# Kernel tuning notes

Hardware: AMD Instinct MI355X
Metric: run time of the kernel (lower is better)

The kernel has to match this reference:

```python
import jax, jax.numpy as jnp
import numpy as np
import math

H = 8        # num_heads
DK = 64      # key_dim
DV = 64      # value_dim
FACTOR = 4


def setup_inputs() -> dict:
    key = jax.random.key(0)
    B, T, S, D = 4, 2048, 2048, 512
    Dout = H * DV
    ks = jax.random.split(key, 16)
    sample_k = min(int(FACTOR * math.log(S)), S)  # = 33
    inp = {
        "x_q": jax.random.normal(ks[0], (B, T, D), jnp.float32),
        "x_k": jax.random.normal(ks[1], (B, S, D), jnp.float32),
        "x_v": jax.random.normal(ks[2], (B, S, D), jnp.float32),
        "Wq": jax.random.normal(ks[3], (D, H * DK), jnp.float32) * 0.02,
        "bq": jnp.zeros((H * DK,), jnp.float32),
        "Wk": jax.random.normal(ks[4], (D, H * DK), jnp.float32) * 0.02,
        "bk": jnp.zeros((H * DK,), jnp.float32),
        "Wv": jax.random.normal(ks[5], (D, H * DV), jnp.float32) * 0.02,
        "bv": jnp.zeros((H * DV,), jnp.float32),
        "Wo": jax.random.normal(ks[6], (H * DV, Dout), jnp.float32) * 0.02,
        "bo": jnp.zeros((Dout,), jnp.float32),
        "index_sample": jax.random.randint(ks[7], (T, sample_k), 0, S, jnp.int32),
    }
    return inp


def reference(x_q, x_k, x_v, Wq, bq, Wk, bk, Wv, bv, Wo, bo, index_sample):
    B, T, D = x_q.shape
    S = x_k.shape[1]
    u = min(int(FACTOR * math.log(T)), T)  # n_top queries kept

    q = (x_q @ Wq + bq).reshape(B, T, H, DK)
    k = (x_k @ Wk + bk).reshape(B, S, H, DK)
    v = (x_v @ Wv + bv).reshape(B, S, H, DV)

    # --- _prob_QK: sampled QK to score queries ---
    ks = k[:, index_sample]                                  # [B,T,J,H,dk]
    qk_s = jnp.einsum('bthd,btjhd->bthj', q, ks)             # [B,T,H,J]
    M = qk_s.max(-1) - qk_s.mean(-1)                         # [B,T,H]
    _, top = jax.lax.top_k(jnp.transpose(M, (0, 2, 1)), u)   # [B,H,u]

    b_idx = jnp.arange(B)[:, None, None]
    h_idx = jnp.arange(H)[None, :, None]
    q_red = q[b_idx, top, h_idx]                             # [B,H,u,dk]
    qk = jnp.einsum('bhud,bshd->bhus', q_red, k)             # [B,H,u,S]

    # --- s0: default (no mask) context = mean of values over S ---
    ctx = jnp.broadcast_to(v.mean(axis=1, keepdims=True), (B, T, H, DV))
    ctx = jnp.transpose(ctx, (0, 2, 1, 3))                   # [B,H,T,dv]

    # --- s1: scaled softmax over full keys for top queries ---
    scores = jax.nn.softmax(qk * (1.0 / math.sqrt(DK)), axis=-1)
    attn = jnp.einsum('bhus,bshd->bhud', scores, v)          # [B,H,u,dv]

    # --- scatter top-query results into context / scores ---
    ctx = ctx.at[b_idx, h_idx, top].set(attn)                # [B,H,T,dv]
    final_scores = jnp.full((B, H, T, S), 1.0 / S, dtype=scores.dtype)
    final_scores = final_scores.at[b_idx, h_idx, top].set(scores)

    out = jnp.transpose(ctx, (0, 2, 1, 3)).reshape(B, T, H * DV)
    out = out @ Wo + bo                                      # [B,T,output_dim]
    return out, final_scores
```

## Files before the change

### kernel.cpp

```cpp
#include <hip/hip_runtime.h>

typedef __attribute__((ext_vector_type(8))) short short8;
typedef __attribute__((ext_vector_type(4))) float f32x4;

constexpr int Bn  = 4;
constexpr int Tn  = 2048;
constexpr int Sn  = 2048;
constexpr int Dn  = 512;
constexpr int Hn  = 8;
constexpr int DKn = 64;
constexpr int DVn = 64;
constexpr int HDn = 512;
constexpr int SKn = 30;
constexpr int Un  = 30;
constexpr int Gu  = 6;
constexpr int NGroups = Un / Gu;
constexpr int NAttnG  = Bn * Hn * NGroups;
constexpr int NOutF   = (Bn * Tn) / 8;
constexpr int RowSplit = 57344;
constexpr int NGemm  = 768;
constexpr int NFillA = RowSplit / 4;
constexpr int NTailF = (Bn * Hn * Tn - RowSplit) / 4;
constexpr float kScale = 0.125f;

constexpr int NWsplit = 192;
constexpr int NVPart  = 64;

__device__ __forceinline__ ushort bf16_rne(float x) {
  unsigned u = __float_as_uint(x);
  return (ushort)((u + 0x7fffu + ((u >> 16) & 1u)) >> 16);
}
__device__ __forceinline__ float bf16f(ushort h) {
  return __uint_as_float(((unsigned)h) << 16);
}
__device__ __forceinline__ void nt_store4(f32x4* p, f32x4 v) {
  __builtin_nontemporal_store(v, p);
}

#define MFMA(accv, av, bv) \
  asm volatile("v_mfma_f32_16x16x32_bf16 %0, %1, %2, %0" : "+v"(accv) : "v"(av), "v"(bv))

__global__ __launch_bounds__(256) void prep_split_kernel(
    const float* __restrict__ Wq, const float* __restrict__ Wk, const float* __restrict__ Wv,
    ushort* __restrict__ WtH, ushort* __restrict__ WtL) {
  const int tid = threadIdx.x;
  const int bid = blockIdx.x;

  const int z = bid / 64, t = bid % 64;
  const int k0 = (t >> 3) * 64, n0 = (t & 7) * 64;
  const float* W = (z == 0) ? Wq : (z == 1) ? Wk : Wv;
  __shared__ float tile[64][65];
  const int r = tid >> 2, c0 = (tid & 3) * 16;
#pragma unroll
  for (int i = 0; i < 16; i += 4) {
    const float4 vv = *(const float4*)(W + (size_t)(k0 + r) * HDn + n0 + c0 + i);
    tile[r][c0 + i] = vv.x; tile[r][c0 + i + 1] = vv.y;
    tile[r][c0 + i + 2] = vv.z; tile[r][c0 + i + 3] = vv.w;
  }
  __syncthreads();
  unsigned hp[8], lp[8];
#pragma unroll
  for (int i = 0; i < 16; i += 2) {
    const float x0 = tile[c0 + i][r];
    const float x1 = tile[c0 + i + 1][r];
    const ushort h0 = bf16_rne(x0), h1 = bf16_rne(x1);
    const ushort l0 = bf16_rne(x0 - bf16f(h0)), l1 = bf16_rne(x1 - bf16f(h1));
    hp[i >> 1] = (unsigned)h0 | ((unsigned)h1 << 16);
    lp[i >> 1] = (unsigned)l0 | ((unsigned)l1 << 16);
  }
  const size_t off = (size_t)(z * 512 + n0 + r) * 512 + k0 + c0;
  *(uint4*)(WtH + off)     = make_uint4(hp[0], hp[1], hp[2], hp[3]);
  *(uint4*)(WtH + off + 8) = make_uint4(hp[4], hp[5], hp[6], hp[7]);
  *(uint4*)(WtL + off)     = make_uint4(lp[0], lp[1], lp[2], lp[3]);
  *(uint4*)(WtL + off + 8) = make_uint4(lp[4], lp[5], lp[6], lp[7]);
}

__global__ __launch_bounds__(256, 2) void gemm_fill_kernel(
    const float* __restrict__ xq, const float* __restrict__ xk, const float* __restrict__ xv,
    const ushort* __restrict__ WtH, const ushort* __restrict__ WtL,
    const float* __restrict__ bq, const float* __restrict__ bk, const float* __restrict__ bv,
    float* __restrict__ qo, float* __restrict__ ko, float* __restrict__ vo,
    float* __restrict__ fscores) {
  const int bid = blockIdx.x;
  const int tid = threadIdx.x;

  if (bid >= NGemm) {
    const size_t r0 = (size_t)(bid - NGemm) * 4;
    const float c = 1.0f / Sn;
    const f32x4 c4v = {c, c, c, c};
    f32x4* fs4 = (f32x4*)fscores + r0 * (Sn / 4);
#pragma unroll
    for (int i = 0; i < 8; ++i) nt_store4(fs4 + i * 256 + tid, c4v);
    return;
  }

  __shared__ ushort AsH[64][32];
  __shared__ ushort AsL[64][32];
  __shared__ ushort BsH[256][32];
  __shared__ ushort BsL[256][32];

  const int z = bid >> 8;
  const int rem = bid & 255;
  const int bm = (rem >> 1) * 64;
  const int bn = (rem & 1) * 256;
  const float* X = (z == 0) ? xq : (z == 1) ? xk : xv;
  const float* bias = (z == 0) ? bq : (z == 1) ? bk : bv;
  float* Y = (z == 0) ? qo : (z == 1) ? ko : vo;

  const int lane = tid & 63;
  const int wave = tid >> 6;
  const int fr = lane & 15;
  const int gk = lane >> 4;

  const int ar = tid >> 2, ag = tid & 3;
  const float* xrow = X + (size_t)(bm + ar) * Dn + ag * 8;
  const int brow0 = tid >> 2, bg = tid & 3;
  const ushort* wh = WtH + (size_t)(z * 512 + bn + brow0) * 512 + bg * 8;
  const ushort* wl = WtL + (size_t)(z * 512 + bn + brow0) * 512 + bg * 8;

  f32x4 acc[4][4];
#pragma unroll
  for (int m = 0; m < 4; ++m)
#pragma unroll
    for (int n = 0; n < 4; ++n)
#pragma unroll
      for (int j = 0; j < 4; ++j) acc[m][n][j] = 0.f;

  float4 af0, af1;
  uint4 sbH[4], sbL[4];
#define STG_LOAD(k0_) do { \
    af0 = *(const float4*)(xrow + (k0_)); \
    af1 = *(const float4*)(xrow + (k0_) + 4); \
    sbH[0] = *(const uint4*)(wh + (k0_));          sbL[0] = *(const uint4*)(wl + (k0_)); \
    sbH[1] = *(const uint4*)(wh + (k0_) + 32768);  sbL[1] = *(const uint4*)(wl + (k0_) + 32768); \
    sbH[2] = *(const uint4*)(wh + (k0_) + 65536);  sbL[2] = *(const uint4*)(wl + (k0_) + 65536); \
    sbH[3] = *(const uint4*)(wh + (k0_) + 98304);  sbL[3] = *(const uint4*)(wl + (k0_) + 98304); \
  } while (0)

  const int agq = (ag ^ ((ar >> 1) & 3)) * 8;
  const int bgx = bg ^ ((brow0 >> 1) & 3);
  const int gq = (gk ^ ((fr >> 1) & 3)) * 8;

  STG_LOAD(0);
  for (int k0 = 0; k0 < Dn; k0 += 32) {
    __syncthreads();
    {
      float xf[8] = {af0.x, af0.y, af0.z, af0.w, af1.x, af1.y, af1.z, af1.w};
      unsigned hp[4], lp[4];
#pragma unroll
      for (int i = 0; i < 8; i += 2) {
        const ushort h0 = bf16_rne(xf[i]), h1 = bf16_rne(xf[i + 1]);
        const ushort l0 = bf16_rne(xf[i] - bf16f(h0)), l1 = bf16_rne(xf[i + 1] - bf16f(h1));
        hp[i >> 1] = (unsigned)h0 | ((unsigned)h1 << 16);
        lp[i >> 1] = (unsigned)l0 | ((unsigned)l1 << 16);
      }
      *(uint4*)&AsH[ar][agq] = make_uint4(hp[0], hp[1], hp[2], hp[3]);
      *(uint4*)&AsL[ar][agq] = make_uint4(lp[0], lp[1], lp[2], lp[3]);
#pragma unroll
      for (int p = 0; p < 4; ++p) {
        const int n = brow0 + p * 64;
        *(uint4*)&BsH[n][bgx * 8] = sbH[p];
        *(uint4*)&BsL[n][bgx * 8] = sbL[p];
      }
    }
    __syncthreads();
    if (k0 + 32 < Dn) STG_LOAD(k0 + 32);

    short8 aH[4], aL[4], bH[4], bL[4];
#pragma unroll
    for (int m = 0; m < 4; ++m) {
      aH[m] = *(const short8*)&AsH[m * 16 + fr][gq];
      aL[m] = *(const short8*)&AsL[m * 16 + fr][gq];
    }
#pragma unroll
    for (int n = 0; n < 4; ++n) {
      bH[n] = *(const short8*)&BsH[wave * 64 + n * 16 + fr][gq];
      bL[n] = *(const short8*)&BsL[wave * 64 + n * 16 + fr][gq];
    }
#pragma unroll
    for (int m = 0; m < 4; ++m)
#pragma unroll
      for (int n = 0; n < 4; ++n) {
        MFMA(acc[m][n], aH[m], bH[n]);
        MFMA(acc[m][n], aH[m], bL[n]);
        MFMA(acc[m][n], aL[m], bH[n]);
      }
  }
  asm volatile("s_nop 7\n\ts_nop 7");

  float bsv[4];
#pragma unroll
  for (int n = 0; n < 4; ++n) bsv[n] = bias[bn + wave * 64 + n * 16 + fr];
#pragma unroll
  for (int m = 0; m < 4; ++m) {
#pragma unroll
    for (int n = 0; n < 4; ++n) {
      const int col = bn + wave * 64 + n * 16 + fr;
#pragma unroll
      for (int j = 0; j < 4; ++j) {
        Y[(size_t)(bm + m * 16 + gk * 4 + j) * HDn + col] = acc[m][n][j] + bsv[n];
      }
    }
  }
#undef STG_LOAD
}

__global__ __launch_bounds__(64) void sampled_m_kernel(
    const float* __restrict__ q, const float* __restrict__ k,
    const int* __restrict__ idxs, float* __restrict__ Mt,
    const float* __restrict__ v, float* __restrict__ vpart) {
  if (blockIdx.x >= Bn * Tn) {
    const int pb = blockIdx.x - Bn * Tn;
    const int b = pb >> 4, part = pb & 15;
    const int ln = threadIdx.x;
    const float4* v4 = (const float4*)(v + (size_t)b * Sn * HDn);
    float4 a0 = make_float4(0.f, 0.f, 0.f, 0.f);
    float4 a1 = make_float4(0.f, 0.f, 0.f, 0.f);
    const int s0 = part * 128;
    for (int s = s0; s < s0 + 128; ++s) {
      const float4 x0 = v4[(size_t)s * 128 + ln * 2];
      const float4 x1 = v4[(size_t)s * 128 + ln * 2 + 1];
      a0.x += x0.x; a0.y += x0.y; a0.z += x0.z; a0.w += x0.w;
      a1.x += x1.x; a1.y += x1.y; a1.z += x1.z; a1.w += x1.w;
    }
    float4* vp4 = (float4*)vpart + (size_t)pb * 128;
    vp4[ln * 2] = a0; vp4[ln * 2 + 1] = a1;
    return;
  }

  const int bt = blockIdx.x;
  const int b = bt >> 11, t = bt & (Tn - 1);
  const int lane = threadIdx.x;
  const int jq = lane >> 4;
  const int d16 = lane & 15;
  __shared__ int sidx[32];
  if (lane < SKn) sidx[lane] = idxs[t * SKn + lane];
  if (lane >= SKn && lane < 32) sidx[lane] = 0;
  __syncthreads();
  const float* qrow = q + (size_t)bt * HDn;
  const float* kb = k + (size_t)b * Sn * HDn;
  for (int h = 0; h < Hn; ++h) {
    const float4 qv = *(const float4*)(qrow + h * DKn + d16 * 4);
    float mx = -1e30f, sum = 0.f;
#pragma unroll
    for (int jb = 0; jb < 32; jb += 4) {
      const int j = jb + jq;
      const int srow = sidx[j];
      const float4 kv = *(const float4*)(kb + (size_t)srow * HDn + h * DKn + d16 * 4);
      float p = kv.x * qv.x + kv.y * qv.y + kv.z * qv.z + kv.w * qv.w;
      p += __shfl_xor(p, 1);
      p += __shfl_xor(p, 2);
      p += __shfl_xor(p, 4);
      p += __shfl_xor(p, 8);
      if (j < SKn) { mx = fmaxf(mx, p); sum += p; }
    }
    mx = fmaxf(mx, __shfl_xor(mx, 16));
    mx = fmaxf(mx, __shfl_xor(mx, 32));
    sum += __shfl_xor(sum, 16);
    sum += __shfl_xor(sum, 32);
    if (lane == 0) Mt[((size_t)(b * Hn + h)) * Tn + t] = mx - sum * (1.0f / SKn);
  }
}

__global__ __launch_bounds__(256) void topk_vmean_base_kernel(
    const float* __restrict__ Mt, const float* __restrict__ vpart,
    const float* __restrict__ Wo, const float* __restrict__ bo,
    int* __restrict__ top, float* __restrict__ vmean, float* __restrict__ basep) {
  const int tid = threadIdx.x;
  const int lane = tid & 63, w = tid >> 6;
  __shared__ float vals[Tn];
  __shared__ float wv[4];
  __shared__ int wi[4];
  __shared__ float4 part[256];
  __shared__ float vm[HDn];

  if (blockIdx.x < 32) {
    const int bh = blockIdx.x;
    for (int i = tid; i < Tn; i += 256) vals[i] = Mt[(size_t)bh * Tn + i];
    __syncthreads();
    for (int u = 0; u < Un; ++u) {
      float bv = -1e30f; int bi = 0x7fffffff;
      for (int i = tid; i < Tn; i += 256) {
        const float x = vals[i];
        if (x > bv) { bv = x; bi = i; }
      }
#pragma unroll
      for (int o = 1; o < 64; o <<= 1) {
        const float ov = __shfl_xor(bv, o);
        const int oi = __shfl_xor(bi, o);
        if (ov > bv || (ov == bv && oi < bi)) { bv = ov; bi = oi; }
      }
      if (lane == 0) { wv[w] = bv; wi[w] = bi; }
      __syncthreads();
      bv = wv[0]; bi = wi[0];
#pragma unroll
      for (int j = 1; j < 4; ++j) {
        if (wv[j] > bv || (wv[j] == bv && wi[j] < bi)) { bv = wv[j]; bi = wi[j]; }
      }
      if (tid == 0) { top[bh * Un + u] = bi; vals[bi] = -1e30f; }
      __syncthreads();
    }
  } else {
    const int b = blockIdx.x - 32;
    const int c4 = tid & 127, half = tid >> 7;
    float4 acc = make_float4(0.f, 0.f, 0.f, 0.f);
    for (int p = half * 8; p < half * 8 + 8; ++p) {
      const float4 x = ((const float4*)vpart)[(size_t)(b * 16 + p) * 128 + c4];
      acc.x += x.x; acc.y += x.y; acc.z += x.z; acc.w += x.w;
    }
    part[tid] = acc;
    __syncthreads();
    if (half == 0) {
      float4 a = part[c4], bpp = part[128 + c4];
      const float sc = 1.0f / Sn;
      float4 r = make_float4((a.x + bpp.x) * sc, (a.y + bpp.y) * sc,
                             (a.z + bpp.z) * sc, (a.w + bpp.w) * sc);
      *(float4*)(vm + c4 * 4) = r;
      *(float4*)(vmean + b * HDn + c4 * 4) = r;
    }
    __syncthreads();
    const float4* Wo4 = (const float4*)Wo;
    float4 acc2 = make_float4(0.f, 0.f, 0.f, 0.f);
    for (int c = half * 256; c < half * 256 + 256; ++c) {
      const float vmc = vm[c];
      const float4 wrow = Wo4[(size_t)c * 128 + c4];
      acc2.x += vmc * wrow.x; acc2.y += vmc * wrow.y;
      acc2.z += vmc * wrow.z; acc2.w += vmc * wrow.w;
    }
    __syncthreads();
    part[tid] = acc2;
    __syncthreads();
    if (half == 0) {
      float4 a = part[c4], bpp = part[128 + c4];
      const float4 bb = ((const float4*)bo)[c4];
      float4 r = make_float4(a.x + bpp.x + bb.x, a.y + bpp.y + bb.y,
                             a.z + bpp.z + bb.z, a.w + bpp.w + bb.w);
      ((float4*)basep)[b * 128 + c4] = r;
    }
  }
}

__global__ __launch_bounds__(256) void attn_out_kernel(
    const float* __restrict__ q, const float* __restrict__ k,
    const float* __restrict__ v, const float* __restrict__ vmean,
    const int* __restrict__ top, const float* __restrict__ Wo,
    const float* __restrict__ basep,
    float* __restrict__ out, float* __restrict__ fscores) {
  const int tid = threadIdx.x;
  const int bid = blockIdx.x;

  if (bid >= NAttnG + NOutF) {
    const int fid = bid - NAttnG - NOutF;
    const int r = RowSplit + fid * 4;
    const int bh = r >> 11;
    const int tbase = r & (Tn - 1);
    __shared__ int sflag4[4];
    if (tid < 4) sflag4[tid] = 0;
    __syncthreads();
    if (tid < Un) {
      const int d = top[bh * Un + tid] - tbase;
      if (d >= 0 && d < 4) sflag4[d] = 1;
    }
    __syncthreads();
    const float c = 1.0f / Sn;
    const f32x4 c4v = {c, c, c, c};
    f32x4* fs4 = (f32x4*)fscores + (size_t)r * (Sn / 4);
#pragma unroll
    for (int rr = 0; rr < 4; ++rr) {
      if (!sflag4[rr]) {
        f32x4* row = fs4 + rr * (Sn / 4);
        nt_store4(row + tid, c4v);
        nt_store4(row + 256 + tid, c4v);
      }
    }
    return;
  }

  if (bid >= NAttnG) {
    const int fid = bid - NAttnG;
    const int r0 = fid * 8;
    const int b = r0 >> 11;
    const int t0 = r0 & (Tn - 1);
    __shared__ int sflag8[8];
    if (tid < 8) sflag8[tid] = 0;
    __syncthreads();
    if (tid < Hn * Un) {
      const int d = top[b * Hn * Un + tid] - t0;
      if (d >= 0 && d < 8) sflag8[d] = 1;
    }
    __syncthreads();
    const int col4 = tid & 127, rh = tid >> 7;
    const float4 bv4 = ((const float4*)basep)[b * 128 + col4];
    const f32x4 bvx = {bv4.x, bv4.y, bv4.z, bv4.w};
#pragma unroll
    for (int rp = 0; rp < 4; ++rp) {
      const int rr = rp * 2 + rh;
      float4* orow4 = (float4*)(out + (size_t)(r0 + rr) * HDn) + col4;
      if (sflag8[rr]) {
        float* p = (float*)orow4;
        atomicAdd(p + 0, bv4.x); atomicAdd(p + 1, bv4.y);
        atomicAdd(p + 2, bv4.z); atomicAdd(p + 3, bv4.w);
      } else {
        nt_store4((f32x4*)orow4, bvx);
      }
    }
    return;
  }

  const int grp = bid % NGroups;
  const int bh = bid / NGroups;
  const int h = bh & (Hn - 1), b = bh >> 3;
  const int u0 = grp * Gu;
  const int lane = tid & 63, w = tid >> 6;

  __shared__ float qs[Gu][DKn];
  __shared__ float sc[Gu][2052];
  __shared__ float red[8];
  __shared__ int tsel[Gu];
  __shared__ float4 partv[4][Gu][16];

  if (tid < Gu) tsel[tid] = top[bh * Un + u0 + tid];
  __syncthreads();
  for (int i = tid; i < Gu * DKn; i += 256) {
    const int g = i >> 6, d = i & 63;
    qs[g][d] = q[((size_t)(b * Tn + tsel[g])) * HDn + h * DKn + d];
  }
  __syncthreads();

  const float4* k4 = (const float4*)k;
  for (int s = tid; s < Sn; s += 256) {
    const float4* krow = k4 + ((size_t)(b * Sn + s)) * 128 + h * 16;
    float acc[Gu];
#pragma unroll
    for (int g = 0; g < Gu; ++g) acc[g] = 0.f;
#pragma unroll
    for (int d4i = 0; d4i < 16; ++d4i) {
      const float4 kv = krow[d4i];
#pragma unroll
      for (int g = 0; g < Gu; ++g) {
        const float4 qv = *(const float4*)&qs[g][d4i * 4];
        acc[g] += kv.x * qv.x + kv.y * qv.y + kv.z * qv.z + kv.w * qv.w;
      }
    }
#pragma unroll
    for (int g = 0; g < Gu; ++g) sc[g][s] = acc[g] * kScale;
  }
  __syncthreads();

  float invs[Gu];
#pragma unroll
  for (int g = 0; g < Gu; ++g) {
    float lm = -1e30f;
    for (int i = tid; i < Sn; i += 256) lm = fmaxf(lm, sc[g][i]);
#pragma unroll
    for (int o = 1; o < 64; o <<= 1) lm = fmaxf(lm, __shfl_xor(lm, o));
    if (lane == 0) red[w] = lm;
    __syncthreads();
    const float mx = fmaxf(fmaxf(red[0], red[1]), fmaxf(red[2], red[3]));
    float ls = 0.f;
    for (int i = tid; i < Sn; i += 256) {
      const float e = __expf(sc[g][i] - mx);
      sc[g][i] = e;
      ls += e;
    }
#pragma unroll
    for (int o = 1; o < 64; o <<= 1) ls += __shfl_xor(ls, o);
    if (lane == 0) red[4 + w] = ls;
    __syncthreads();
    invs[g] = 1.0f / (red[4] + red[5] + red[6] + red[7]);
    __syncthreads();
  }
#pragma unroll
  for (int g = 0; g < Gu; ++g) {
    const float inv = invs[g];
    float4* scg4 = (float4*)sc[g];
    f32x4* fsrow4 = (f32x4*)(fscores + ((size_t)bh * Tn + tsel[g]) * Sn);
#pragma unroll
    for (int it = 0; it < 2; ++it) {
      const int i = it * 256 + tid;
      float4 p = scg4[i];
      p.x *= inv; p.y *= inv; p.z *= inv; p.w *= inv;
      scg4[i] = p;
      const f32x4 px = {p.x, p.y, p.z, p.w};
      nt_store4(fsrow4 + i, px);
    }
  }
  __syncthreads();

  const int d4 = lane & 15;
  const int sg = (w << 2) + (lane >> 4);
  const float4* v4 = (const float4*)v;
  float4 pacc[Gu];
#pragma unroll
  for (int g = 0; g < Gu; ++g) pacc[g] = make_float4(0.f, 0.f, 0.f, 0.f);
  for (int s = sg; s < Sn; s += 16) {
    const float4 vv = v4[((size_t)(b * Sn + s)) * 128 + h * 16 + d4];
#pragma unroll
    for (int g = 0; g < Gu; ++g) {
      const float p = sc[g][s];
      pacc[g].x += p * vv.x; pacc[g].y += p * vv.y;
      pacc[g].z += p * vv.z; pacc[g].w += p * vv.w;
    }
  }
#pragma unroll
  for (int g = 0; g < Gu; ++g) {
#pragma unroll
    for (int o = 16; o < 64; o <<= 1) {
      pacc[g].x += __shfl_xor(pacc[g].x, o);
      pacc[g].y += __shfl_xor(pacc[g].y, o);
      pacc[g].z += __shfl_xor(pacc[g].z, o);
      pacc[g].w += __shfl_xor(pacc[g].w, o);
    }
    if (lane < 16) partv[w][g][lane] = pacc[g];
  }
  __syncthreads();
  if (tid < Gu * 16) {
    const int g = tid >> 4, dd = tid & 15;
    float4 r = partv[0][g][dd];
    const float4 r1 = partv[1][g][dd], r2 = partv[2][g][dd], r3 = partv[3][g][dd];
    r.x += r1.x + r2.x + r3.x; r.y += r1.y + r2.y + r3.y;
    r.z += r1.z + r2.z + r3.z; r.w += r1.w + r2.w + r3.w;
    const float4 vm4 = ((const float4*)vmean)[bh * 16 + dd];
    r.x -= vm4.x; r.y -= vm4.y; r.z -= vm4.z; r.w -= vm4.w;
    *(float4*)&qs[g][dd * 4] = r;
  }
  __syncthreads();

  const int col4 = tid & 127, gg = tid >> 7;
  const float4* Wo4 = (const float4*)Wo;
#pragma unroll
  for (int gp = 0; gp < Gu / 2; ++gp) {
    const int g = gp * 2 + gg;
    float4 a = make_float4(0.f, 0.f, 0.f, 0.f);
#pragma unroll
    for (int d = 0; d < DKn; ++d) {
      const float dv = qs[g][d];
      const float4 wrow = Wo4[(size_t)(h * DKn + d) * 128 + col4];
      a.x += dv * wrow.x; a.y += dv * wrow.y;
      a.z += dv * wrow.z; a.w += dv * wrow.w;
    }
    float* orow = out + ((size_t)(b * Tn + tsel[g])) * HDn + col4 * 4;
    atomicAdd(orow + 0, a.x); atomicAdd(orow + 1, a.y);
    atomicAdd(orow + 2, a.z); atomicAdd(orow + 3, a.w);
  }
}

extern "C" void kernel_launch(void* const* d_in, const int* in_sizes, int n_in,
                              void* d_out, int out_size, void* d_ws, size_t ws_size,
                              hipStream_t stream) {
  const float* x_q = (const float*)d_in[0];
  const float* x_k = (const float*)d_in[1];
  const float* x_v = (const float*)d_in[2];
  const float* Wq = (const float*)d_in[3];
  const float* bq = (const float*)d_in[4];
  const float* Wk = (const float*)d_in[5];
  const float* bk = (const float*)d_in[6];
  const float* Wv = (const float*)d_in[7];
  const float* bv = (const float*)d_in[8];
  const float* Wo = (const float*)d_in[9];
  const float* bo = (const float*)d_in[10];
  const int* idx = (const int*)d_in[11];

  float* out = (float*)d_out;
  float* fscores = out + (size_t)Bn * Tn * HDn;

  float* ws = (float*)d_ws;
  float* q = ws;
  float* kp = ws + (size_t)4194304;
  float* vp = ws + (size_t)8388608;
  float* Mt = ws + (size_t)12582912;
  float* vmean = ws + (size_t)12648448;
  float* basep = ws + (size_t)12650496;
  int* top = (int*)(ws + (size_t)12652544);

  char* scr = (char*)(fscores + (size_t)RowSplit * Sn);
  ushort* WtH = (ushort*)scr;
  ushort* WtL = WtH + (size_t)3 * 512 * 512;
  float* vpart = (float*)(WtL + (size_t)3 * 512 * 512);

  prep_split_kernel<<<NWsplit, 256, 0, stream>>>(Wq, Wk, Wv, WtH, WtL);

  gemm_fill_kernel<<<NGemm + NFillA, 256, 0, stream>>>(
      x_q, x_k, x_v, WtH, WtL, bq, bk, bv, q, kp, vp, fscores);

  sampled_m_kernel<<<Bn * Tn + NVPart, 64, 0, stream>>>(q, kp, idx, Mt, vp, vpart);

  topk_vmean_base_kernel<<<36, 256, 0, stream>>>(Mt, vpart, Wo, bo, top, vmean, basep);

  attn_out_kernel<<<NAttnG + NOutF + NTailF, 256, 0, stream>>>(
      q, kp, vp, vmean, top, Wo, basep, out, fscores);
}
```

Measured before the change: 898.7 us.

## Move score fill into sampled kernel, widen K loads, swizzle block order

The uniform 1/S fill of final_scores is moved out of the GEMM kernel and the attention-tail blocks into the sampled-M kernel, which now fills every row before the attention kernel overwrites the top rows. This overlaps the large store stream with the latency-bound sampled gather instead of with the compute-heavy GEMM, and removes the per-row top-flag checks in the tail fill. The sampled-M kernel now uses 8 lanes per key row with two float4 loads each. Block indices in both the sampled and attention kernels are remapped to interleave batches, aiming for better cache locality. vpart moves into the workspace because the fill now overwrites the scratch area inside fscores that used to hold it. The cost is a little redundant writing of rows that are later overwritten.

After: 910.5 us. Within noise of the previous version (+1.3%).

```diff
diff --git a/kernel.cpp b/kernel.cpp
--- a/kernel.cpp
+++ b/kernel.cpp
@@ -17,14 +17,13 @@
 constexpr int NGroups = Un / Gu;
 constexpr int NAttnG  = Bn * Hn * NGroups;
 constexpr int NOutF   = (Bn * Tn) / 8;
-constexpr int RowSplit = 57344;
 constexpr int NGemm  = 768;
-constexpr int NFillA = RowSplit / 4;
-constexpr int NTailF = (Bn * Hn * Tn - RowSplit) / 4;
 constexpr float kScale = 0.125f;
 
 constexpr int NWsplit = 192;
 constexpr int NVPart  = 64;
+constexpr int NSampled = Bn * Tn;
+constexpr int NFillS  = (Bn * Hn * Tn) / 4;
 
 __device__ __forceinline__ ushort bf16_rne(float x) {
   unsigned u = __float_as_uint(x);
@@ -75,24 +74,13 @@
   *(uint4*)(WtL + off + 8) = make_uint4(lp[4], lp[5], lp[6], lp[7]);
 }
 
-__global__ __launch_bounds__(256, 2) void gemm_fill_kernel(
+__global__ __launch_bounds__(256, 2) void gemm_kernel(
     const float* __restrict__ xq, const float* __restrict__ xk, const float* __restrict__ xv,
     const ushort* __restrict__ WtH, const ushort* __restrict__ WtL,
     const float* __restrict__ bq, const float* __restrict__ bk, const float* __restrict__ bv,
-    float* __restrict__ qo, float* __restrict__ ko, float* __restrict__ vo,
-    float* __restrict__ fscores) {
+    float* __restrict__ qo, float* __restrict__ ko, float* __restrict__ vo) {
   const int bid = blockIdx.x;
   const int tid = threadIdx.x;
-
-  if (bid >= NGemm) {
-    const size_t r0 = (size_t)(bid - NGemm) * 4;
-    const float c = 1.0f / Sn;
-    const f32x4 c4v = {c, c, c, c};
-    f32x4* fs4 = (f32x4*)fscores + r0 * (Sn / 4);
-#pragma unroll
-    for (int i = 0; i < 8; ++i) nt_store4(fs4 + i * 256 + tid, c4v);
-    return;
-  }
 
   __shared__ ushort AsH[64][32];
   __shared__ ushort AsL[64][32];
@@ -208,54 +196,74 @@
 __global__ __launch_bounds__(64) void sampled_m_kernel(
     const float* __restrict__ q, const float* __restrict__ k,
     const int* __restrict__ idxs, float* __restrict__ Mt,
-    const float* __restrict__ v, float* __restrict__ vpart) {
-  if (blockIdx.x >= Bn * Tn) {
-    const int pb = blockIdx.x - Bn * Tn;
+    const float* __restrict__ v, float* __restrict__ vpart,
+    float* __restrict__ fscores) {
+  const int bid = blockIdx.x;
+  const int lane = threadIdx.x;
+
+  if (bid >= NVPart + NSampled) {
+    const size_t fb = (size_t)(bid - NVPart - NSampled);
+    const float c = 1.0f / Sn;
+    const f32x4 c4v = {c, c, c, c};
+    f32x4* p = (f32x4*)fscores + fb * 2048;
+#pragma unroll
+    for (int i = 0; i < 32; ++i) nt_store4(p + i * 64 + lane, c4v);
+    return;
+  }
+
+  if (bid < NVPart) {
+    const int pb = bid;
     const int b = pb >> 4, part = pb & 15;
-    const int ln = threadIdx.x;
     const float4* v4 = (const float4*)(v + (size_t)b * Sn * HDn);
     float4 a0 = make_float4(0.f, 0.f, 0.f, 0.f);
     float4 a1 = make_float4(0.f, 0.f, 0.f, 0.f);
     const int s0 = part * 128;
     for (int s = s0; s < s0 + 128; ++s) {
-      const float4 x0 = v4[(size_t)s * 128 + ln * 2];
-      const float4 x1 = v4[(size_t)s * 128 + ln * 2 + 1];
+      const float4 x0 = v4[(size_t)s * 128 + lane * 2];
+      const float4 x1 = v4[(size_t)s * 128 + lane * 2 + 1];
       a0.x += x0.x; a0.y += x0.y; a0.z += x0.z; a0.w += x0.w;
       a1.x += x1.x; a1.y += x1.y; a1.z += x1.z; a1.w += x1.w;
     }
     float4* vp4 = (float4*)vpart + (size_t)pb * 128;
-    vp4[ln * 2] = a0; vp4[ln * 2 + 1] = a1;
+    vp4[lane * 2] = a0; vp4[lane * 2 + 1] = a1;
     return;
   }
 
-  const int bt = blockIdx.x;
-  const int b = bt >> 11, t = bt & (Tn - 1);
-  const int lane = threadIdx.x;
-  const int jq = lane >> 4;
-  const int d16 = lane & 15;
+  const int inner = bid - NVPart;
+  const int x = inner & 7;
+  const int b = x & 3;
+  const int t = ((inner >> 3) << 1) | (x >> 2);
+
+  const int sg = lane >> 3;
+  const int d8 = lane & 7;
   __shared__ int sidx[32];
   if (lane < SKn) sidx[lane] = idxs[t * SKn + lane];
   if (lane >= SKn && lane < 32) sidx[lane] = 0;
   __syncthreads();
-  const float* qrow = q + (size_t)bt * HDn;
+  const float* qrow = q + ((size_t)(b * Tn + t)) * HDn;
   const float* kb = k + (size_t)b * Sn * HDn;
   for (int h = 0; h < Hn; ++h) {
-    const float4 qv = *(const float4*)(qrow + h * DKn + d16 * 4);
+    const float4 qv0 = *(const float4*)(qrow + h * DKn + d8 * 8);
+    const float4 qv1 = *(const float4*)(qrow + h * DKn + d8 * 8 + 4);
     float mx = -1e30f, sum = 0.f;
 #pragma unroll
-    for (int jb = 0; jb < 32; jb += 4) {
-      const int j = jb + jq;
+    for (int jb = 0; jb < 32; jb += 8) {
+      const int j = jb + sg;
       const int srow = sidx[j];
-      const float4 kv = *(const float4*)(kb + (size_t)srow * HDn + h * DKn + d16 * 4);
-      float p = kv.x * qv.x + kv.y * qv.y + kv.z * qv.z + kv.w * qv.w;
+      const float* kr = kb + (size_t)srow * HDn + h * DKn + d8 * 8;
+      const float4 kv0 = *(const float4*)kr;
+      const float4 kv1 = *(const float4*)(kr + 4);
+      float p = kv0.x * qv0.x + kv0.y * qv0.y + kv0.z * qv0.z + kv0.w * qv0.w
+              + kv1.x * qv1.x + kv1.y * qv1.y + kv1.z * qv1.z + kv1.w * qv1.w;
       p += __shfl_xor(p, 1);
       p += __shfl_xor(p, 2);
       p += __shfl_xor(p, 4);
-      p += __shfl_xor(p, 8);
       if (j < SKn) { mx = fmaxf(mx, p); sum += p; }
     }
+    mx = fmaxf(mx, __shfl_xor(mx, 8));
     mx = fmaxf(mx, __shfl_xor(mx, 16));
     mx = fmaxf(mx, __shfl_xor(mx, 32));
+    sum += __shfl_xor(sum, 8);
     sum += __shfl_xor(sum, 16);
     sum += __shfl_xor(sum, 32);
     if (lane == 0) Mt[((size_t)(b * Hn + h)) * Tn + t] = mx - sum * (1.0f / SKn);
@@ -349,33 +357,6 @@
   const int tid = threadIdx.x;
   const int bid = blockIdx.x;
 
-  if (bid >= NAttnG + NOutF) {
-    const int fid = bid - NAttnG - NOutF;
-    const int r = RowSplit + fid * 4;
-    const int bh = r >> 11;
-    const int tbase = r & (Tn - 1);
-    __shared__ int sflag4[4];
-    if (tid < 4) sflag4[tid] = 0;
-    __syncthreads();
-    if (tid < Un) {
-      const int d = top[bh * Un + tid] - tbase;
-      if (d >= 0 && d < 4) sflag4[d] = 1;
-    }
-    __syncthreads();
-    const float c = 1.0f / Sn;
-    const f32x4 c4v = {c, c, c, c};
-    f32x4* fs4 = (f32x4*)fscores + (size_t)r * (Sn / 4);
-#pragma unroll
-    for (int rr = 0; rr < 4; ++rr) {
-      if (!sflag4[rr]) {
-        f32x4* row = fs4 + rr * (Sn / 4);
-        nt_store4(row + tid, c4v);
-        nt_store4(row + 256 + tid, c4v);
-      }
-    }
-    return;
-  }
-
   if (bid >= NAttnG) {
     const int fid = bid - NAttnG;
     const int r0 = fid * 8;
@@ -407,9 +388,12 @@
     return;
   }
 
-  const int grp = bid % NGroups;
-  const int bh = bid / NGroups;
-  const int h = bh & (Hn - 1), b = bh >> 3;
+  const int xs = bid & 7;
+  const int b = xs & 3;
+  const int combo = (bid >> 3) + (xs >> 2) * 20;
+  const int h = combo / 5;
+  const int grp = combo % 5;
+  const int bh = b * Hn + h;
   const int u0 = grp * Gu;
   const int lane = tid & 63, w = tid >> 6;
 
@@ -572,21 +556,22 @@
   float* vmean = ws + (size_t)12648448;
   float* basep = ws + (size_t)12650496;
   int* top = (int*)(ws + (size_t)12652544);
-
-  char* scr = (char*)(fscores + (size_t)RowSplit * Sn);
+  float* vpart = ws + (size_t)12656640;
+
+  char* scr = (char*)(fscores + (size_t)49152 * Sn);
   ushort* WtH = (ushort*)scr;
   ushort* WtL = WtH + (size_t)3 * 512 * 512;
-  float* vpart = (float*)(WtL + (size_t)3 * 512 * 512);
 
   prep_split_kernel<<<NWsplit, 256, 0, stream>>>(Wq, Wk, Wv, WtH, WtL);
 
-  gemm_fill_kernel<<<NGemm + NFillA, 256, 0, stream>>>(
-      x_q, x_k, x_v, WtH, WtL, bq, bk, bv, q, kp, vp, fscores);
-
-  sampled_m_kernel<<<Bn * Tn + NVPart, 64, 0, stream>>>(q, kp, idx, Mt, vp, vpart);
+  gemm_kernel<<<NGemm, 256, 0, stream>>>(
+      x_q, x_k, x_v, WtH, WtL, bq, bk, bv, q, kp, vp);
+
+  sampled_m_kernel<<<NVPart + NSampled + NFillS, 64, 0, stream>>>(
+      q, kp, idx, Mt, vp, vpart, fscores);
 
   topk_vmean_base_kernel<<<36, 256, 0, stream>>>(Mt, vpart, Wo, bo, top, vmean, basep);
 
-  attn_out_kernel<<<NAttnG + NOutF + NTailF, 256, 0, stream>>>(
+  attn_out_kernel<<<NAttnG + NOutF, 256, 0, stream>>>(
       q, kp, vp, vmean, top, Wo, basep, out, fscores);
 }
```
